# Kernel optimization log

Hardware: AMD Instinct MI355X
Metric: run time of the kernel (lower is better)

## Reference

```python
import jax, jax.numpy as jnp
import numpy as np

D_MODEL = 1024
D_K = 1024
B, T = 4, 2048


def setup_inputs() -> dict:
    key = jax.random.key(0)
    kx, kq, kk, kv = jax.random.split(key, 4)
    s = 1.0 / np.sqrt(D_MODEL)
    return {
        "x": jax.random.normal(kx, (B, T, D_MODEL), dtype=jnp.float32),
        "W_q": jax.random.normal(kq, (D_MODEL, D_K), dtype=jnp.float32) * s,
        "W_k": jax.random.normal(kk, (D_MODEL, D_K), dtype=jnp.float32) * s,
        "W_v": jax.random.normal(kv, (D_MODEL, D_K), dtype=jnp.float32) * s,
    }


def reference(x, W_q, W_k, W_v):
    # x: (B, T, C); W_*: (C, d_k). Linear(no bias) == x @ W
    q = jnp.einsum('btc,ck->btk', x, W_q)
    k = jnp.einsum('btc,ck->btk', x, W_k)
    v = jnp.einsum('btc,ck->btk', x, W_v)
    d_k = W_q.shape[1]
    scores = jnp.einsum('bqk,bsk->bqs', q, k) / jnp.sqrt(jnp.asarray(d_k, x.dtype))
    T_ = x.shape[1]
    causal = jnp.tril(jnp.ones((T_, T_), dtype=bool))
    scores = jnp.where(causal, scores, jnp.asarray(-jnp.inf, scores.dtype))
    weights = jax.nn.softmax(scores, axis=-1)
    return jnp.einsum('bqs,bsk->bqk', weights, v)
```

## Files before the change

### kernel.cpp

```cpp
#include <hip/hip_runtime.h>
#include <hip/hip_bf16.h>
#include <stdint.h>
#include <math.h>

typedef __bf16 bf16x8 __attribute__((ext_vector_type(8)));
typedef float  f32x4  __attribute__((ext_vector_type(4)));
typedef unsigned int u32x4 __attribute__((ext_vector_type(4)));

__device__ __forceinline__ unsigned short f2bf(float x) {
    union { float f; unsigned u; } v; v.f = x;
    unsigned r = v.u + 0x7fffu + ((v.u >> 16) & 1u);
    return (unsigned short)(r >> 16);
}

__device__ __forceinline__ float bf2f(unsigned short b) {
    union { unsigned u; float f; } v; v.u = ((unsigned)b) << 16; return v.f;
}

__device__ __forceinline__ void async16(const void* g, void* l) {
    __builtin_amdgcn_global_load_lds(
        (const __attribute__((address_space(1))) void*)g,
        (__attribute__((address_space(3))) void*)l,
        16, 0, 0);
}

template <typename OutT, bool KLIMIT, bool VFOLD, int ZMODE>
__global__ __launch_bounds__(256, 3) void gemm_bt(
    const unsigned short* __restrict__ A,
    const unsigned short* __restrict__ Bt,
    OutT* __restrict__ C,
    unsigned short* __restrict__ VtOut,
    int M, int N, int K, int lda, int ldb, int ldc,
    int ldvt, int nsplit,
    long long sA, long long sB, long long sC, long long sVt, float scale)
{
    int bn, bm, bz;
    if constexpr (ZMODE == 1) {
        const int o = blockIdx.x, x = o & 7, q = o >> 3;
        bz = x >> 1;
        const int tile = (x & 1) * 192 + q * 4 + blockIdx.z;
        bn = tile / 16; bm = tile % 16;
    } else if constexpr (ZMODE == 2) {
        const int o = blockIdx.x, x = o & 7, q = o >> 3;
        bz = x >> 1;
        const int t = (x & 1) * 68 + q * 4 + blockIdx.z;
        int r = (int)((sqrtf(8.f * (float)t + 1.f) - 1.f) * 0.5f);
        while ((r + 1) * (r + 2) / 2 <= t) r++;
        while (r * (r + 1) / 2 > t) r--;
        bm = r; bn = t - r * (r + 1) / 2;
    } else if constexpr (ZMODE == 3) {
        const int o = blockIdx.x, x = o & 7, q = o >> 3;
        bz = x >> 1;
        const int tile = (x & 1) * 64 + q * 4 + blockIdx.z;
        bn = tile >> 4; bm = 15 - (tile & 15);
    } else {
        bn = blockIdx.x;
        bm = KLIMIT ? (gridDim.y - 1 - blockIdx.y) : blockIdx.y;
        bz = blockIdx.z;
    }

    A  += (long long)bz * sA;
    Bt += (long long)bz * sB;
    C  += (long long)bz * sC;

    const int m0 = bm * 128, n0 = bn * 128;
    const int Keff = KLIMIT ? min(K, (bm + 1) * 128) : K;
    const int nsteps = Keff >> 5;

    __shared__ __align__(16) unsigned short LDS[3 * 8192];

    const int tid  = threadIdx.x;
    const int w    = tid >> 6, l = tid & 63;
    const int wr   = w >> 1,  wc = w & 1;
    const int lrow = l & 15,  quad = l >> 4;

    f32x4 acc[4][4] = {};

    const int rA0  = 32 * w + (l >> 2);
    const int cOff = (((l & 3) ^ ((l >> 3) & 3))) * 8;
    const unsigned short* aG0 = A  + (long long)(m0 + rA0)      * lda + cOff;
    const unsigned short* aG1 = A  + (long long)(m0 + rA0 + 16) * lda + cOff;
    const unsigned short* bG0 = Bt + (long long)(n0 + rA0)      * ldb + cOff;
    const unsigned short* bG1 = Bt + (long long)(n0 + rA0 + 16) * ldb + cOff;
    unsigned short* aL = &LDS[(2 * w) * 512 + l * 8];
    unsigned short* bL = aL + 4096;

    const int sl = (lrow >> 1) & 3;

    auto STG = [&](int s) {
        const int off = (s % 3) * 8192;
        const int kk  = s * 32;
        async16(aG0 + kk, aL + off);
        async16(aG1 + kk, aL + off + 512);
        async16(bG0 + kk, bL + off);
        async16(bG1 + kk, bL + off + 512);
    };

    STG(0);
    if (nsteps > 1) STG(1);

    for (int t = 0; t < nsteps; ++t) {
        if (t + 1 < nsteps) asm volatile("s_waitcnt vmcnt(4)" ::: "memory");
        else                asm volatile("s_waitcnt vmcnt(0)" ::: "memory");
        __builtin_amdgcn_s_barrier();
        asm volatile("" ::: "memory");

        if (t + 2 < nsteps) STG(t + 2);

        const unsigned short* As = &LDS[(t % 3) * 8192];
        const unsigned short* Bs = As + 4096;
        bf16x8 af[4], bfr[4];
#pragma unroll
        for (int i = 0; i < 4; i++) {
            af[i]  = *(const bf16x8*)&As[(wr * 64 + i * 16 + lrow) * 32 + (quad ^ sl) * 8];
            bfr[i] = *(const bf16x8*)&Bs[(wc * 64 + i * 16 + lrow) * 32 + (quad ^ sl) * 8];
        }
#pragma unroll
        for (int i = 0; i < 4; i++)
#pragma unroll
            for (int j = 0; j < 4; j++)
                acc[i][j] = __builtin_amdgcn_mfma_f32_16x16x32_bf16(af[i], bfr[j], acc[i][j], 0, 0, 0);
    }

    if constexpr (VFOLD) {
        if (n0 >= nsplit) {
            unsigned short* Vp = VtOut + (long long)bz * sVt;
#pragma unroll
            for (int i = 0; i < 4; i++) {
                const int t = m0 + wr * 64 + i * 16 + quad * 4;
#pragma unroll
                for (int j = 0; j < 4; j++) {
                    const int d = (n0 - nsplit) + wc * 64 + j * 16 + lrow;
                    union { unsigned short u[4]; uint2 p; } o;
#pragma unroll
                    for (int r = 0; r < 4; r++) o.u[r] = f2bf(acc[i][j][r] * scale);
                    *(uint2*)(Vp + (long long)d * ldvt + t) = o.p;
                }
            }
            return;
        }
    }

    __syncthreads();

    char* eb = (char*)LDS + w * 2288;
    const int erow = l >> 2, ep = l & 3;

    if constexpr (sizeof(OutT) == 2) {
#pragma unroll
        for (int i = 0; i < 4; i++) {
#pragma unroll
            for (int j = 0; j < 4; j++)
#pragma unroll
                for (int r = 0; r < 4; r++)
                    *(unsigned short*)(eb + (quad * 4 + r) * 144 + (j * 16 + lrow) * 2) =
                        f2bf(acc[i][j][r] * scale);
            const long long gm = m0 + wr * 64 + i * 16 + erow;
#pragma unroll
            for (int c = 0; c < 2; c++) {
                u32x4 d = *(u32x4*)(eb + erow * 144 + ep * 32 + c * 16);
                *(u32x4*)((unsigned short*)C + gm * ldc + (n0 + wc * 64 + ep * 16 + c * 8)) = d;
            }
        }
    } else {
#pragma unroll
        for (int i = 0; i < 4; i++) {
            const long long gm = m0 + wr * 64 + i * 16 + erow;
#pragma unroll
            for (int jc = 0; jc < 2; jc++) {
#pragma unroll
                for (int jj = 0; jj < 2; jj++)
#pragma unroll
                    for (int r = 0; r < 4; r++)
                        *(float*)(eb + (quad * 4 + r) * 144 + (jj * 16 + lrow) * 4) =
                            acc[i][2 * jc + jj][r] * scale;
#pragma unroll
                for (int c = 0; c < 2; c++) {
                    f32x4 d = *(f32x4*)(eb + erow * 144 + ep * 32 + c * 16);
                    *(f32x4*)((float*)C + gm * ldc + (n0 + wc * 64 + jc * 32 + ep * 8 + c * 4)) = d;
                }
            }
        }
    }
}

__global__ __launch_bounds__(256) void prep_fused(
    const float4* __restrict__ xin, unsigned short* __restrict__ xout, int n4, int nCast,
    const float* __restrict__ W0, const float* __restrict__ W1,
    const float* __restrict__ W2, unsigned short* __restrict__ wout, int n)
{
    const int tid = threadIdx.x;
    if ((int)blockIdx.x < nCast) {
        int i = blockIdx.x * 256 + tid;
        if (i >= n4) return;
        float4 v = xin[i];
        union { unsigned short u[4]; uint2 p; } o;
        o.u[0] = f2bf(v.x); o.u[1] = f2bf(v.y); o.u[2] = f2bf(v.z); o.u[3] = f2bf(v.w);
        *(uint2*)(xout + (long long)i * 4) = o.p;
        return;
    }
    const int bx = blockIdx.x - nCast;
    const int wz = bx >> 10, rem = bx & 1023;
    const int wy = rem >> 5, wx = rem & 31;
    const float* in = (wz == 0) ? W0 : (wz == 1) ? W1 : W2;
    unsigned short* out = wout + (long long)wz * n * n;
    __shared__ float tile[32][33];
    const int tx = tid & 31, ty = tid >> 5;
    const int c0 = wx * 32, r0 = wy * 32;
#pragma unroll
    for (int i = 0; i < 4; i++)
        tile[ty + i * 8][tx] = in[(long long)(r0 + ty + i * 8) * n + c0 + tx];
    __syncthreads();
#pragma unroll
    for (int i = 0; i < 4; i++)
        out[(long long)(c0 + ty + i * 8) * n + r0 + tx] = f2bf(tile[tx][ty + i * 8]);
}

__global__ __launch_bounds__(256) void causal_softmax_bf16(
    const unsigned short* __restrict__ S, unsigned short* __restrict__ P, int T)
{
    const int row = blockIdx.x;
    const int t   = row & (T - 1);
    const int L   = t + 1;
    const unsigned short* s = S + (long long)row * T;
    unsigned short* p = P + (long long)row * T;
    const int tid  = threadIdx.x;
    const int base = tid * 8;

    uint4 raw = *(const uint4*)(s + base);
    unsigned rr[4] = {raw.x, raw.y, raw.z, raw.w};
    float v[8];
#pragma unroll
    for (int k = 0; k < 4; k++) {
        union { unsigned u; float f; } a, b;
        a.u = (rr[k] & 0xFFFFu) << 16;
        b.u = rr[k] & 0xFFFF0000u;
        v[2 * k] = a.f; v[2 * k + 1] = b.f;
    }
    float mx = -3.0e38f;
#pragma unroll
    for (int k = 0; k < 8; k++) {
        if (base + k >= L) v[k] = -3.0e38f;
        mx = fmaxf(mx, v[k]);
    }
#pragma unroll
    for (int off = 32; off; off >>= 1) mx = fmaxf(mx, __shfl_xor(mx, off));
    __shared__ float red[4], red2[4];
    const int wid = tid >> 6, lid = tid & 63;
    if (lid == 0) red[wid] = mx;
    __syncthreads();
    mx = fmaxf(fmaxf(red[0], red[1]), fmaxf(red[2], red[3]));

    float sum = 0.f;
#pragma unroll
    for (int k = 0; k < 8; k++) { v[k] = __expf(v[k] - mx); sum += v[k]; }
#pragma unroll
    for (int off = 32; off; off >>= 1) sum += __shfl_xor(sum, off);
    if (lid == 0) red2[wid] = sum;
    __syncthreads();
    sum = red2[0] + red2[1] + red2[2] + red2[3];
    const float inv = 1.0f / sum;

    union { unsigned short u[8]; uint4 q; } o;
#pragma unroll
    for (int k = 0; k < 8; k++) o.u[k] = f2bf(v[k] * inv);
    *(uint4*)(p + base) = o.q;
}

extern "C" void kernel_launch(void* const* d_in, const int* in_sizes, int n_in,
                              void* d_out, int out_size, void* d_ws, size_t ws_size,
                              hipStream_t stream)
{
    const int B = 4, T = 2048, C = 1024, D = 1024;
    const float* x  = (const float*)d_in[0];
    const float* Wq = (const float*)d_in[1];
    const float* Wk = (const float*)d_in[2];
    const float* Wv = (const float*)d_in[3];
    float* out = (float*)d_out;
    char* ws = (char*)d_ws;

    const size_t MB = 1ull << 20;
    unsigned short* Xbf   = (unsigned short*)(ws + 0);
    unsigned short* WqkvT = (unsigned short*)(ws + 16 * MB);
    unsigned short* QK    = (unsigned short*)(ws + 22 * MB);
    unsigned short* Vt    = (unsigned short*)(ws + 54 * MB);
    unsigned short* Sbf   = (unsigned short*)(ws + 70 * MB);
    unsigned short* P     = (unsigned short*)(ws + 0);

    const long long sX  = (long long)T * C;
    const long long sQK = (long long)T * 2 * D;
    const long long sVt = (long long)D * T;
    const long long sS  = (long long)T * T;
    const long long sO  = (long long)T * D;

    {
        int n4 = B * T * C / 4;
        int nCast = (n4 + 255) / 256;
        prep_fused<<<dim3(nCast + 3072), dim3(256), 0, stream>>>(
            (const float4*)x, Xbf, n4, nCast, Wq, Wk, Wv, WqkvT, 1024);
    }
    {
        dim3 g(384, 1, 4), b(256);
        gemm_bt<unsigned short, false, true, 1><<<g, b, 0, stream>>>(
            Xbf, WqkvT, QK, Vt, 2048, 3072, 1024, 1024, 1024, 2048,
             T,  2048, sX, 0, sQK, sVt, 1.0f);
    }
    {
        dim3 g(136, 1, 4), b(256);
        gemm_bt<unsigned short, false, false, 2><<<g, b, 0, stream>>>(
            QK, QK + D, Sbf, nullptr, 2048, 2048, 1024, 2 * D, 2 * D, 2048,
            0, 0, sQK, sQK, sS, 0, 0.03125f);
    }
    {
        causal_softmax_bf16<<<dim3(B * T), dim3(256), 0, stream>>>(Sbf, P, T);
    }
    {
        dim3 g(128, 1, 4), b(256);
        gemm_bt<float, true, false, 3><<<g, b, 0, stream>>>(
            P, Vt, out, nullptr, 2048, 1024, 2048, 2048, 2048, 1024,
            0, 0, sS, sVt, sO, 0, 1.0f);
    }
    (void)in_sizes; (void)n_in; (void)out_size; (void)ws_size;
}
```

Baseline: 233.0 us.

## Widen GEMM tiles to 128x256 to double B-operand reuse per block

Doubles the N dimension of each GEMM block tile from 128 to 256. Each wave now holds a 4x8 accumulator array and the LDS stage buffers grow to hold the wider B tile. Tile-index mappings for the QKV, score and PV launches are redone for the halved grids, including a new triangular enumeration for the causal score GEMM. The aim is higher arithmetic intensity and fewer A-tile reloads. The cost is more registers and LDS, lower occupancy (launch bounds drop from 3 to 2 blocks), fewer blocks for load balance, and coarser causal skipping at 128x256 granularity.

Result: slower. 244.5 us (+4.9%).

```diff
diff --git a/kernel.cpp b/kernel.cpp
--- a/kernel.cpp
+++ b/kernel.cpp
@@ -25,7 +25,7 @@
 }
 
 template <typename OutT, bool KLIMIT, bool VFOLD, int ZMODE>
-__global__ __launch_bounds__(256, 3) void gemm_bt(
+__global__ __launch_bounds__(256, 2) void gemm_bt(
     const unsigned short* __restrict__ A,
     const unsigned short* __restrict__ Bt,
     OutT* __restrict__ C,
@@ -38,87 +38,88 @@
     if constexpr (ZMODE == 1) {
         const int o = blockIdx.x, x = o & 7, q = o >> 3;
         bz = x >> 1;
-        const int tile = (x & 1) * 192 + q * 4 + blockIdx.z;
+        const int tile = (x & 1) * 96 + q * 4 + blockIdx.z;
         bn = tile / 16; bm = tile % 16;
     } else if constexpr (ZMODE == 2) {
         const int o = blockIdx.x, x = o & 7, q = o >> 3;
         bz = x >> 1;
-        const int t = (x & 1) * 68 + q * 4 + blockIdx.z;
-        int r = (int)((sqrtf(8.f * (float)t + 1.f) - 1.f) * 0.5f);
-        while ((r + 1) * (r + 2) / 2 <= t) r++;
-        while (r * (r + 1) / 2 > t) r--;
-        bm = r; bn = t - r * (r + 1) / 2;
+        const int t = (x & 1) * 36 + q * 4 + blockIdx.z;
+        int acc2 = 0; bm = 0;
+        while (acc2 + (bm / 2 + 1) <= t) { acc2 += bm / 2 + 1; bm++; }
+        bn = t - acc2;
     } else if constexpr (ZMODE == 3) {
         const int o = blockIdx.x, x = o & 7, q = o >> 3;
         bz = x >> 1;
-        const int tile = (x & 1) * 64 + q * 4 + blockIdx.z;
+        const int tile = (x & 1) * 32 + q * 4 + blockIdx.z;
         bn = tile >> 4; bm = 15 - (tile & 15);
     } else {
-        bn = blockIdx.x;
-        bm = KLIMIT ? (gridDim.y - 1 - blockIdx.y) : blockIdx.y;
-        bz = blockIdx.z;
+        bn = blockIdx.x; bm = blockIdx.y; bz = blockIdx.z;
     }
 
     A  += (long long)bz * sA;
     Bt += (long long)bz * sB;
     C  += (long long)bz * sC;
 
-    const int m0 = bm * 128, n0 = bn * 128;
+    const int m0 = bm * 128, n0 = bn * 256;
     const int Keff = KLIMIT ? min(K, (bm + 1) * 128) : K;
     const int nsteps = Keff >> 5;
 
-    __shared__ __align__(16) unsigned short LDS[3 * 8192];
+    __shared__ __align__(16) unsigned short LDS[3 * 12288];
 
     const int tid  = threadIdx.x;
     const int w    = tid >> 6, l = tid & 63;
     const int wr   = w >> 1,  wc = w & 1;
     const int lrow = l & 15,  quad = l >> 4;
 
-    f32x4 acc[4][4] = {};
-
-    const int rA0  = 32 * w + (l >> 2);
+    f32x4 acc[4][8] = {};
+
     const int cOff = (((l & 3) ^ ((l >> 3) & 3))) * 8;
-    const unsigned short* aG0 = A  + (long long)(m0 + rA0)      * lda + cOff;
-    const unsigned short* aG1 = A  + (long long)(m0 + rA0 + 16) * lda + cOff;
-    const unsigned short* bG0 = Bt + (long long)(n0 + rA0)      * ldb + cOff;
-    const unsigned short* bG1 = Bt + (long long)(n0 + rA0 + 16) * ldb + cOff;
-    unsigned short* aL = &LDS[(2 * w) * 512 + l * 8];
-    unsigned short* bL = aL + 4096;
+    const unsigned short* aG0 = A  + (long long)(m0 + 32 * w + (l >> 2))      * lda + cOff;
+    const unsigned short* aG1 = A  + (long long)(m0 + 32 * w + (l >> 2) + 16) * lda + cOff;
+    const unsigned short* bG0 = Bt + (long long)(n0 + 64 * w + (l >> 2))      * ldb + cOff;
+    const unsigned short* bG1 = Bt + (long long)(n0 + 64 * w + (l >> 2) + 16) * ldb + cOff;
+    const unsigned short* bG2 = Bt + (long long)(n0 + 64 * w + (l >> 2) + 32) * ldb + cOff;
+    const unsigned short* bG3 = Bt + (long long)(n0 + 64 * w + (l >> 2) + 48) * ldb + cOff;
+    unsigned short* aL = &LDS[w * 1024 + l * 8];
+    unsigned short* bL = &LDS[4096 + w * 2048 + l * 8];
 
     const int sl = (lrow >> 1) & 3;
 
     auto STG = [&](int s) {
-        const int off = (s % 3) * 8192;
+        const int off = (s % 3) * 12288;
         const int kk  = s * 32;
         async16(aG0 + kk, aL + off);
         async16(aG1 + kk, aL + off + 512);
         async16(bG0 + kk, bL + off);
         async16(bG1 + kk, bL + off + 512);
+        async16(bG2 + kk, bL + off + 1024);
+        async16(bG3 + kk, bL + off + 1536);
     };
 
     STG(0);
     if (nsteps > 1) STG(1);
 
     for (int t = 0; t < nsteps; ++t) {
-        if (t + 1 < nsteps) asm volatile("s_waitcnt vmcnt(4)" ::: "memory");
+        if (t + 1 < nsteps) asm volatile("s_waitcnt vmcnt(6)" ::: "memory");
         else                asm volatile("s_waitcnt vmcnt(0)" ::: "memory");
         __builtin_amdgcn_s_barrier();
         asm volatile("" ::: "memory");
 
         if (t + 2 < nsteps) STG(t + 2);
 
-        const unsigned short* As = &LDS[(t % 3) * 8192];
+        const unsigned short* As = &LDS[(t % 3) * 12288];
         const unsigned short* Bs = As + 4096;
-        bf16x8 af[4], bfr[4];
-#pragma unroll
-        for (int i = 0; i < 4; i++) {
+        bf16x8 af[4], bfr[8];
+#pragma unroll
+        for (int i = 0; i < 4; i++)
             af[i]  = *(const bf16x8*)&As[(wr * 64 + i * 16 + lrow) * 32 + (quad ^ sl) * 8];
-            bfr[i] = *(const bf16x8*)&Bs[(wc * 64 + i * 16 + lrow) * 32 + (quad ^ sl) * 8];
-        }
+#pragma unroll
+        for (int j = 0; j < 8; j++)
+            bfr[j] = *(const bf16x8*)&Bs[(wc * 128 + j * 16 + lrow) * 32 + (quad ^ sl) * 8];
 #pragma unroll
         for (int i = 0; i < 4; i++)
 #pragma unroll
-            for (int j = 0; j < 4; j++)
+            for (int j = 0; j < 8; j++)
                 acc[i][j] = __builtin_amdgcn_mfma_f32_16x16x32_bf16(af[i], bfr[j], acc[i][j], 0, 0, 0);
     }
 
@@ -129,8 +130,8 @@
             for (int i = 0; i < 4; i++) {
                 const int t = m0 + wr * 64 + i * 16 + quad * 4;
 #pragma unroll
-                for (int j = 0; j < 4; j++) {
-                    const int d = (n0 - nsplit) + wc * 64 + j * 16 + lrow;
+                for (int j = 0; j < 8; j++) {
+                    const int d = (n0 - nsplit) + wc * 128 + j * 16 + lrow;
                     union { unsigned short u[4]; uint2 p; } o;
 #pragma unroll
                     for (int r = 0; r < 4; r++) o.u[r] = f2bf(acc[i][j][r] * scale);
@@ -143,31 +144,32 @@
 
     __syncthreads();
 
-    char* eb = (char*)LDS + w * 2288;
     const int erow = l >> 2, ep = l & 3;
 
     if constexpr (sizeof(OutT) == 2) {
+        char* eb = (char*)LDS + w * 4352;
 #pragma unroll
         for (int i = 0; i < 4; i++) {
 #pragma unroll
-            for (int j = 0; j < 4; j++)
+            for (int j = 0; j < 8; j++)
 #pragma unroll
                 for (int r = 0; r < 4; r++)
-                    *(unsigned short*)(eb + (quad * 4 + r) * 144 + (j * 16 + lrow) * 2) =
+                    *(unsigned short*)(eb + (quad * 4 + r) * 272 + (j * 16 + lrow) * 2) =
                         f2bf(acc[i][j][r] * scale);
             const long long gm = m0 + wr * 64 + i * 16 + erow;
 #pragma unroll
-            for (int c = 0; c < 2; c++) {
-                u32x4 d = *(u32x4*)(eb + erow * 144 + ep * 32 + c * 16);
-                *(u32x4*)((unsigned short*)C + gm * ldc + (n0 + wc * 64 + ep * 16 + c * 8)) = d;
+            for (int c = 0; c < 4; c++) {
+                u32x4 d = *(u32x4*)(eb + erow * 272 + ep * 64 + c * 16);
+                *(u32x4*)((unsigned short*)C + gm * ldc + (n0 + wc * 128 + ep * 32 + c * 8)) = d;
             }
         }
     } else {
+        char* eb = (char*)LDS + w * 2304;
 #pragma unroll
         for (int i = 0; i < 4; i++) {
             const long long gm = m0 + wr * 64 + i * 16 + erow;
 #pragma unroll
-            for (int jc = 0; jc < 2; jc++) {
+            for (int jc = 0; jc < 4; jc++) {
 #pragma unroll
                 for (int jj = 0; jj < 2; jj++)
 #pragma unroll
@@ -177,7 +179,7 @@
 #pragma unroll
                 for (int c = 0; c < 2; c++) {
                     f32x4 d = *(f32x4*)(eb + erow * 144 + ep * 32 + c * 16);
-                    *(f32x4*)((float*)C + gm * ldc + (n0 + wc * 64 + jc * 32 + ep * 8 + c * 4)) = d;
+                    *(f32x4*)((float*)C + gm * ldc + (n0 + wc * 128 + jc * 32 + ep * 8 + c * 4)) = d;
                 }
             }
         }
@@ -300,13 +302,13 @@
             (const float4*)x, Xbf, n4, nCast, Wq, Wk, Wv, WqkvT, 1024);
     }
     {
-        dim3 g(384, 1, 4), b(256);
+        dim3 g(192, 1, 4), b(256);
         gemm_bt<unsigned short, false, true, 1><<<g, b, 0, stream>>>(
             Xbf, WqkvT, QK, Vt, 2048, 3072, 1024, 1024, 1024, 2048,
              T,  2048, sX, 0, sQK, sVt, 1.0f);
     }
     {
-        dim3 g(136, 1, 4), b(256);
+        dim3 g(72, 1, 4), b(256);
         gemm_bt<unsigned short, false, false, 2><<<g, b, 0, stream>>>(
             QK, QK + D, Sbf, nullptr, 2048, 2048, 1024, 2 * D, 2 * D, 2048,
             0, 0, sQK, sQK, sS, 0, 0.03125f);
@@ -315,7 +317,7 @@
         causal_softmax_bf16<<<dim3(B * T), dim3(256), 0, stream>>>(Sbf, P, T);
     }
     {
-        dim3 g(128, 1, 4), b(256);
+        dim3 g(64, 1, 4), b(256);
         gemm_bt<float, true, false, 3><<<g, b, 0, stream>>>(
             P, Vt, out, nullptr, 2048, 1024, 2048, 2048, 2048, 1024,
             0, 0, sS, sVt, sO, 0, 1.0f);
```
